# Kernel tuning notes

Measured on AMD Instinct MI355X. Metric: run time of the kernel, lower is better.

The kernel has to match this reference:

```python
import jax, jax.numpy as jnp
import numpy as np

N_NODES = 100000
N_EDGES = 3200000
N_FEAT = 512
HIDDEN = 16
N_CLASSES = 40


def gcn_conv(x, src, dst, W, b, num_nodes):
    # GCNConv with self-loops and symmetric normalization (default PyG settings).
    loop = jnp.arange(num_nodes)
    s = jnp.concatenate([src, loop])
    d = jnp.concatenate([dst, loop])
    deg = jax.ops.segment_sum(jnp.ones_like(s, dtype=x.dtype), d, num_segments=num_nodes)
    dinv = jnp.where(deg > 0, jax.lax.rsqrt(deg), 0.0)
    norm = dinv[s] * dinv[d]  # [E+N]
    h = x @ W  # [N, out]
    msg = h[s] * norm[:, None]  # gather + scale
    out = jax.ops.segment_sum(msg, d, num_segments=num_nodes)  # scatter-add
    return out + b


def setup_inputs() -> dict:
    key = jax.random.key(0)
    k1, k2, k3, k4 = jax.random.split(key, 4)
    x = jax.random.normal(k1, (N_NODES, N_FEAT), dtype=jnp.float32)
    edge_index = jax.random.randint(k2, (2, N_EDGES), 0, N_NODES, dtype=jnp.int64)
    W1 = jax.random.normal(k3, (N_FEAT, HIDDEN), dtype=jnp.float32) * 0.05
    b1 = jnp.zeros((HIDDEN,), dtype=jnp.float32)
    W2 = jax.random.normal(k4, (HIDDEN, N_CLASSES), dtype=jnp.float32) * 0.05
    b2 = jnp.zeros((N_CLASSES,), dtype=jnp.float32)
    return {"x": x, "edge_index": edge_index, "W1": W1, "b1": b1, "W2": W2, "b2": b2}


def reference(x, edge_index, W1, b1, W2, b2):
    num_nodes = x.shape[0]
    src, dst = edge_index[0], edge_index[1]
    h = gcn_conv(x, src, dst, W1, b1, num_nodes)
    h = jax.nn.relu(h)
    # dropout is identity in eval mode (training=False)
    out = gcn_conv(h, src, dst, W2, b2, num_nodes)
    return jax.nn.log_softmax(out, axis=1)
```

## Files before the change

kernel.cpp:

```cpp
#include <hip/hip_runtime.h>

#define N_NODES 100000
#define N_EDGES 3200000
#define N_FEAT 512
#define HIDDEN 16
#define N_CLASSES 40

#define SCAN_BLOCKS 98


__global__ void k_zero_int(int* p, int n) {
    int i = blockIdx.x * 256 + threadIdx.x;
    if (i < n) p[i] = 0;
}

__global__ void k_count(const int* __restrict__ dst, int* __restrict__ cnt,
                        int* __restrict__ ord) {
    int e = blockIdx.x * 256 + threadIdx.x;
    if (e < N_EDGES) ord[e] = atomicAdd(cnt + dst[e], 1);
}

__global__ void k_dinv(const int* __restrict__ cnt, float* __restrict__ dinv) {
    int i = blockIdx.x * 256 + threadIdx.x;
    if (i < N_NODES) dinv[i] = rsqrtf((float)(cnt[i] + 1));
}


__global__ __launch_bounds__(1024) void k_scan_a(const int* __restrict__ cnt,
                                                 int* __restrict__ bsum) {
    int tid = threadIdx.x;
    int i = blockIdx.x * 1024 + tid;
    int v = (i < N_NODES) ? cnt[i] : 0;
    #pragma unroll
    for (int off = 32; off >= 1; off >>= 1) v += __shfl_xor(v, off, 64);
    __shared__ int ws[16];
    if ((tid & 63) == 0) ws[tid >> 6] = v;
    __syncthreads();
    if (tid == 0) {
        int s = 0;
        #pragma unroll
        for (int w = 0; w < 16; w++) s += ws[w];
        bsum[blockIdx.x] = s;
    }
}

__global__ __launch_bounds__(128) void k_scan_b(const int* __restrict__ bsum,
                                                int* __restrict__ boff) {
    int tid = threadIdx.x;
    int lane = tid & 63, wv = tid >> 6;
    int v = (tid < SCAN_BLOCKS) ? bsum[tid] : 0;
    int sc = v;
    #pragma unroll
    for (int off = 1; off < 64; off <<= 1) {
        int t = __shfl_up(sc, off, 64);
        if (lane >= off) sc += t;
    }
    __shared__ int wsum[2];
    if (lane == 63) wsum[wv] = sc;
    __syncthreads();
    int pre = (wv == 1) ? wsum[0] : 0;
    if (tid < SCAN_BLOCKS) boff[tid] = pre + sc - v;
}

__global__ __launch_bounds__(1024) void k_scan_c(const int* __restrict__ cnt,
                                                 const int* __restrict__ boff,
                                                 int* __restrict__ row_start) {
    int tid = threadIdx.x;
    int i = blockIdx.x * 1024 + tid;
    int lane = tid & 63, wv = tid >> 6;
    int v = (i < N_NODES) ? cnt[i] : 0;
    int sc = v;
    #pragma unroll
    for (int off = 1; off < 64; off <<= 1) {
        int t = __shfl_up(sc, off, 64);
        if (lane >= off) sc += t;
    }
    __shared__ int wsum[16];
    if (lane == 63) wsum[wv] = sc;
    __syncthreads();
    int pre = 0;
    #pragma unroll
    for (int w = 0; w < 16; w++) pre += (w < wv) ? wsum[w] : 0;
    int excl = boff[blockIdx.x] + pre + sc - v;
    if (i < N_NODES) row_start[i] = excl;
    if (i == N_NODES) row_start[N_NODES] = N_EDGES;
}

__global__ void k_build(const int* __restrict__ src, const int* __restrict__ dst,
                        const int* __restrict__ ord, const int* __restrict__ row_start,
                        const float* __restrict__ dinv, int2* __restrict__ edge_data) {
    int e = blockIdx.x * 256 + threadIdx.x;
    if (e >= N_EDGES) return;
    int s = src[e], d = dst[e];
    int slot = row_start[d] + ord[e];
    float nrm = dinv[s] * dinv[d];
    edge_data[slot] = make_int2(s, __float_as_int(nrm));
}


#define KC 32
#define LDSW 36

__global__ __launch_bounds__(256) void k_gemm1(const float* __restrict__ x,
                                               const float* __restrict__ W1,
                                               float* __restrict__ h1) {
    __shared__ float xs[256 * LDSW];
    int tid = threadIdx.x;
    int row = blockIdx.x * 256 + tid;

    float acc[HIDDEN];
    #pragma unroll
    for (int j = 0; j < HIDDEN; j++) acc[j] = 0.f;

    int s_sub = tid >> 3;
    int s_k4  = tid & 7;

    for (int kc = 0; kc < N_FEAT; kc += KC) {
        __syncthreads();
        #pragma unroll
        for (int l = 0; l < 8; l++) {
            int srow = s_sub + l * 32;
            int grow = blockIdx.x * 256 + srow;
            int gr = grow < N_NODES ? grow : N_NODES - 1;
            float4 v = *reinterpret_cast<const float4*>(
                x + (size_t)gr * N_FEAT + kc + s_k4 * 4);
            *reinterpret_cast<float4*>(&xs[srow * LDSW + s_k4 * 4]) = v;
        }
        __syncthreads();

        const float* Wc = W1 + kc * HIDDEN;
        #pragma unroll
        for (int k4 = 0; k4 < 8; k4++) {
            float4 xv = *reinterpret_cast<const float4*>(&xs[tid * LDSW + k4 * 4]);
            const float* w0 = Wc + (k4 * 4 + 0) * HIDDEN;
            const float* w1 = Wc + (k4 * 4 + 1) * HIDDEN;
            const float* w2 = Wc + (k4 * 4 + 2) * HIDDEN;
            const float* w3 = Wc + (k4 * 4 + 3) * HIDDEN;
            #pragma unroll
            for (int j = 0; j < HIDDEN; j++) {
                acc[j] += xv.x * w0[j];
                acc[j] += xv.y * w1[j];
                acc[j] += xv.z * w2[j];
                acc[j] += xv.w * w3[j];
            }
        }
    }

    if (row < N_NODES) {
        float4* op = reinterpret_cast<float4*>(h1 + (size_t)row * HIDDEN);
        #pragma unroll
        for (int q = 0; q < 4; q++)
            op[q] = make_float4(acc[q*4+0], acc[q*4+1], acc[q*4+2], acc[q*4+3]);
    }
}


template <bool RELU>
__global__ __launch_bounds__(256) void k_agg16(const int2* __restrict__ edge_data,
                                               const int* __restrict__ row_start,
                                               const float* __restrict__ dinv,
                                               const float* __restrict__ h,
                                               const float* __restrict__ bias,
                                               float* __restrict__ out) {
    int g = threadIdx.x >> 4, j = threadIdx.x & 15;
    int node = blockIdx.x * 16 + g;
    if (node >= N_NODES) return;
    int beg = row_start[node], end = row_start[node + 1];
    float ds = dinv[node];
    float acc = h[(size_t)node * HIDDEN + j] * (ds * ds);
    int i = beg;
    for (; i + 3 < end; i += 4) {
        int2 e0 = edge_data[i + 0];
        int2 e1 = edge_data[i + 1];
        int2 e2 = edge_data[i + 2];
        int2 e3 = edge_data[i + 3];
        float v0 = h[(size_t)e0.x * HIDDEN + j];
        float v1 = h[(size_t)e1.x * HIDDEN + j];
        float v2 = h[(size_t)e2.x * HIDDEN + j];
        float v3 = h[(size_t)e3.x * HIDDEN + j];
        acc += v0 * __int_as_float(e0.y);
        acc += v1 * __int_as_float(e1.y);
        acc += v2 * __int_as_float(e2.y);
        acc += v3 * __int_as_float(e3.y);
    }
    for (; i < end; ++i) {
        int2 ed = edge_data[i];
        acc += h[(size_t)ed.x * HIDDEN + j] * __int_as_float(ed.y);
    }
    if (RELU) acc = fmaxf(acc + bias[j], 0.f);
    out[(size_t)node * HIDDEN + j] = acc;
}


__global__ __launch_bounds__(256) void k_out(const float* __restrict__ agg2,
                                             const float* __restrict__ W2,
                                             const float* __restrict__ b2,
                                             float* __restrict__ out) {
    int r = blockIdx.x * 256 + threadIdx.x;
    if (r >= N_NODES) return;
    float a[HIDDEN];
    const float4* ap = reinterpret_cast<const float4*>(agg2 + (size_t)r * HIDDEN);
    #pragma unroll
    for (int q = 0; q < 4; q++) {
        float4 v = ap[q];
        a[q * 4 + 0] = v.x; a[q * 4 + 1] = v.y;
        a[q * 4 + 2] = v.z; a[q * 4 + 3] = v.w;
    }
    float acc[N_CLASSES];
    #pragma unroll
    for (int jj = 0; jj < N_CLASSES; jj++) acc[jj] = b2[jj];
    #pragma unroll
    for (int kk = 0; kk < HIDDEN; kk++) {
        float av = a[kk];
        #pragma unroll
        for (int jj = 0; jj < N_CLASSES; jj++)
            acc[jj] += av * W2[kk * N_CLASSES + jj];
    }
    float m = -1e30f;
    #pragma unroll
    for (int jj = 0; jj < N_CLASSES; jj++) m = fmaxf(m, acc[jj]);
    float sum = 0.f;
    #pragma unroll
    for (int jj = 0; jj < N_CLASSES; jj++) sum += __expf(acc[jj] - m);
    float l = m + __logf(sum);
    float4* op = reinterpret_cast<float4*>(out + (size_t)r * N_CLASSES);
    #pragma unroll
    for (int q = 0; q < N_CLASSES / 4; q++) {
        op[q] = make_float4(acc[q*4+0] - l, acc[q*4+1] - l,
                            acc[q*4+2] - l, acc[q*4+3] - l);
    }
}


extern "C" void kernel_launch(void* const* d_in, const int* in_sizes, int n_in,
                              void* d_out, int out_size, void* d_ws, size_t ws_size,
                              hipStream_t stream) {
    const float* x  = (const float*)d_in[0];
    const int*   ei = (const int*)d_in[1];
    const float* W1 = (const float*)d_in[2];
    const float* b1 = (const float*)d_in[3];
    const float* W2 = (const float*)d_in[4];
    const float* b2 = (const float*)d_in[5];
    const int* src = ei;
    const int* dst = ei + N_EDGES;
    float* out = (float*)d_out;

    char* ws = (char*)d_ws;
    size_t off = 0;
    auto alloc = [&](size_t bytes) {
        size_t o = off; off = (off + bytes + 255) & ~(size_t)255; return o;
    };
    float* dinv      = (float*)(ws + alloc(sizeof(float) * N_NODES));
    int*   cnt       = (int*)  (ws + alloc(sizeof(int) * N_NODES));
    int*   row_start = (int*)  (ws + alloc(sizeof(int) * (N_NODES + 1)));
    int*   ord       = (int*)  (ws + alloc(sizeof(int) * N_EDGES));
    int2*  edge_data = (int2*) (ws + alloc(sizeof(int2) * N_EDGES));
    float* h1        = (float*)(ws + alloc(sizeof(float) * N_NODES * HIDDEN));
    float* rbuf      = (float*)(ws + alloc(sizeof(float) * N_NODES * HIDDEN));
    float* agg2      = (float*)(ws + alloc(sizeof(float) * N_NODES * HIDDEN));
    int*   bsum      = (int*)  (ws + alloc(sizeof(int) * SCAN_BLOCKS));
    int*   boff      = (int*)  (ws + alloc(sizeof(int) * SCAN_BLOCKS));

    const int nodeBlocks  = (N_NODES + 255) / 256;
    const int edgeBlocks  = (N_EDGES + 255) / 256;
    const int aggBlocks   = (N_NODES + 15) / 16;

    k_zero_int<<<nodeBlocks, 256, 0, stream>>>(cnt, N_NODES);
    k_count<<<edgeBlocks, 256, 0, stream>>>(dst, cnt, ord);
    k_dinv<<<nodeBlocks, 256, 0, stream>>>(cnt, dinv);
    k_scan_a<<<SCAN_BLOCKS, 1024, 0, stream>>>(cnt, bsum);
    k_scan_b<<<1, 128, 0, stream>>>(bsum, boff);
    k_scan_c<<<SCAN_BLOCKS, 1024, 0, stream>>>(cnt, boff, row_start);
    k_build<<<edgeBlocks, 256, 0, stream>>>(src, dst, ord, row_start, dinv, edge_data);

    k_gemm1<<<nodeBlocks, 256, 0, stream>>>(x, W1, h1);
    k_agg16<true><<<aggBlocks, 256, 0, stream>>>(edge_data, row_start, dinv, h1, b1, rbuf);
    k_agg16<false><<<aggBlocks, 256, 0, stream>>>(edge_data, row_start, dinv, rbuf, nullptr, agg2);
    k_out<<<nodeBlocks, 256, 0, stream>>>(agg2, W2, b2, out);
}
```

Measured before the change: 677.1 us.

## Privatize degree counters per XCD with workgroup-scope atomics

```diff
diff --git a/kernel.cpp b/kernel.cpp
--- a/kernel.cpp
+++ b/kernel.cpp
@@ -5,6 +5,7 @@
 #define N_FEAT 512
 #define HIDDEN 16
 #define N_CLASSES 40
+#define NXCD 8
 
 #define SCAN_BLOCKS 98
 
@@ -14,15 +15,36 @@
     if (i < n) p[i] = 0;
 }
 
-__global__ void k_count(const int* __restrict__ dst, int* __restrict__ cnt,
+__device__ __forceinline__ int xcc_id() {
+    int x;
+    asm("s_getreg_b32 %0, hwreg(HW_REG_XCC_ID)" : "=s"(x));
+    return x & (NXCD - 1);
+}
+
+__global__ void k_count(const int* __restrict__ dst, int* __restrict__ cnt8,
                         int* __restrict__ ord) {
     int e = blockIdx.x * 256 + threadIdx.x;
-    if (e < N_EDGES) ord[e] = atomicAdd(cnt + dst[e], 1);
-}
-
-__global__ void k_dinv(const int* __restrict__ cnt, float* __restrict__ dinv) {
+    if (e >= N_EDGES) return;
+    int c = xcc_id();
+    int d = dst[e];
+    int o = __hip_atomic_fetch_add(cnt8 + c * N_NODES + d, 1,
+                                   __ATOMIC_RELAXED, __HIP_MEMORY_SCOPE_WORKGROUP);
+    ord[e] = (o << 3) | c;
+}
+
+__global__ void k_merge(int* __restrict__ cnt8, int* __restrict__ cnt,
+                        float* __restrict__ dinv) {
     int i = blockIdx.x * 256 + threadIdx.x;
-    if (i < N_NODES) dinv[i] = rsqrtf((float)(cnt[i] + 1));
+    if (i >= N_NODES) return;
+    int s = 0;
+    #pragma unroll
+    for (int c = 0; c < NXCD; c++) {
+        int v = cnt8[c * N_NODES + i];
+        cnt8[c * N_NODES + i] = s;
+        s += v;
+    }
+    cnt[i] = s;
+    dinv[i] = rsqrtf((float)(s + 1));
 }
 
 
@@ -88,11 +110,14 @@
 
 __global__ void k_build(const int* __restrict__ src, const int* __restrict__ dst,
                         const int* __restrict__ ord, const int* __restrict__ row_start,
-                        const float* __restrict__ dinv, int2* __restrict__ edge_data) {
+                        const int* __restrict__ cnt8, const float* __restrict__ dinv,
+                        int2* __restrict__ edge_data) {
     int e = blockIdx.x * 256 + threadIdx.x;
     if (e >= N_EDGES) return;
     int s = src[e], d = dst[e];
-    int slot = row_start[d] + ord[e];
+    int oc = ord[e];
+    int c = oc & (NXCD - 1), o = oc >> 3;
+    int slot = row_start[d] + cnt8[c * N_NODES + d] + o;
     float nrm = dinv[s] * dinv[d];
     edge_data[slot] = make_int2(s, __float_as_int(nrm));
 }
@@ -260,18 +285,20 @@
     float* agg2      = (float*)(ws + alloc(sizeof(float) * N_NODES * HIDDEN));
     int*   bsum      = (int*)  (ws + alloc(sizeof(int) * SCAN_BLOCKS));
     int*   boff      = (int*)  (ws + alloc(sizeof(int) * SCAN_BLOCKS));
+    int*   cnt8      = (int*)agg2;
 
     const int nodeBlocks  = (N_NODES + 255) / 256;
     const int edgeBlocks  = (N_EDGES + 255) / 256;
     const int aggBlocks   = (N_NODES + 15) / 16;
-
-    k_zero_int<<<nodeBlocks, 256, 0, stream>>>(cnt, N_NODES);
-    k_count<<<edgeBlocks, 256, 0, stream>>>(dst, cnt, ord);
-    k_dinv<<<nodeBlocks, 256, 0, stream>>>(cnt, dinv);
+    const int zero8Blocks = (NXCD * N_NODES + 255) / 256;
+
+    k_zero_int<<<zero8Blocks, 256, 0, stream>>>(cnt8, NXCD * N_NODES);
+    k_count<<<edgeBlocks, 256, 0, stream>>>(dst, cnt8, ord);
+    k_merge<<<nodeBlocks, 256, 0, stream>>>(cnt8, cnt, dinv);
     k_scan_a<<<SCAN_BLOCKS, 1024, 0, stream>>>(cnt, bsum);
     k_scan_b<<<1, 128, 0, stream>>>(bsum, boff);
     k_scan_c<<<SCAN_BLOCKS, 1024, 0, stream>>>(cnt, boff, row_start);
-    k_build<<<edgeBlocks, 256, 0, stream>>>(src, dst, ord, row_start, dinv, edge_data);
+    k_build<<<edgeBlocks, 256, 0, stream>>>(src, dst, ord, row_start, cnt8, dinv, edge_data);
 
     k_gemm1<<<nodeBlocks, 256, 0, stream>>>(x, W1, h1);
     k_agg16<true><<<aggBlocks, 256, 0, stream>>>(edge_data, row_start, dinv, h1, b1, rbuf);
```

New measurement: 690.7 us. 1.02x slower.

## Build CSR with LDS-partitioned histogram counting and bucketed placement

Applied to the files above, without the earlier changes.

```diff
diff --git a/kernel.cpp b/kernel.cpp
--- a/kernel.cpp
+++ b/kernel.cpp
@@ -8,21 +8,49 @@
 
 #define SCAN_BLOCKS 98
 
-
-__global__ void k_zero_int(int* p, int n) {
-    int i = blockIdx.x * 256 + threadIdx.x;
-    if (i < n) p[i] = 0;
-}
-
-__global__ void k_count(const int* __restrict__ dst, int* __restrict__ cnt,
-                        int* __restrict__ ord) {
-    int e = blockIdx.x * 256 + threadIdx.x;
-    if (e < N_EDGES) ord[e] = atomicAdd(cnt + dst[e], 1);
-}
-
-__global__ void k_dinv(const int* __restrict__ cnt, float* __restrict__ dinv) {
-    int i = blockIdx.x * 256 + threadIdx.x;
-    if (i < N_NODES) dinv[i] = rsqrtf((float)(cnt[i] + 1));
+#define CH    16384
+#define NCH   7
+#define NS    32
+#define SLICE (N_EDGES / NS)
+#define SL4   (SLICE / 4)
+
+__global__ __launch_bounds__(512) void k_p1(const int* __restrict__ dst,
+                                            int* __restrict__ partS) {
+    __shared__ int hist[CH];
+    int tid = threadIdx.x;
+    int s = blockIdx.x, j = blockIdx.y;
+    int base = j * CH;
+    int lim = N_NODES - base; if (lim > CH) lim = CH;
+    for (int i = tid; i < CH; i += 512) hist[i] = 0;
+    __syncthreads();
+    const int4* dp = reinterpret_cast<const int4*>(dst + s * SLICE);
+    for (int i = tid; i < SL4; i += 512) {
+        int4 d4 = dp[i];
+        unsigned a = (unsigned)(d4.x - base); if (a < (unsigned)lim) atomicAdd(&hist[a], 1);
+        unsigned b = (unsigned)(d4.y - base); if (b < (unsigned)lim) atomicAdd(&hist[b], 1);
+        unsigned c = (unsigned)(d4.z - base); if (c < (unsigned)lim) atomicAdd(&hist[c], 1);
+        unsigned d = (unsigned)(d4.w - base); if (d < (unsigned)lim) atomicAdd(&hist[d], 1);
+    }
+    __syncthreads();
+    for (int i = tid; i < lim; i += 512)
+        partS[s * N_NODES + base + i] = hist[i];
+}
+
+__global__ __launch_bounds__(256) void k_colscan(int* __restrict__ partS,
+                                                 int* __restrict__ deg,
+                                                 float* __restrict__ dinv) {
+    int n = blockIdx.x * 256 + threadIdx.x;
+    if (n >= N_NODES) return;
+    int run = 0;
+    #pragma unroll
+    for (int s = 0; s < NS; s++) {
+        int idx = s * N_NODES + n;
+        int v = partS[idx];
+        partS[idx] = run;
+        run += v;
+    }
+    deg[n] = run;
+    dinv[n] = rsqrtf((float)(run + 1));
 }
 
 
@@ -86,15 +114,54 @@
     if (i == N_NODES) row_start[N_NODES] = N_EDGES;
 }
 
-__global__ void k_build(const int* __restrict__ src, const int* __restrict__ dst,
-                        const int* __restrict__ ord, const int* __restrict__ row_start,
-                        const float* __restrict__ dinv, int2* __restrict__ edge_data) {
-    int e = blockIdx.x * 256 + threadIdx.x;
-    if (e >= N_EDGES) return;
-    int s = src[e], d = dst[e];
-    int slot = row_start[d] + ord[e];
-    float nrm = dinv[s] * dinv[d];
-    edge_data[slot] = make_int2(s, __float_as_int(nrm));
+__global__ __launch_bounds__(512) void k_p2(const int* __restrict__ src,
+                                            const int* __restrict__ dst,
+                                            const int* __restrict__ partS,
+                                            const int* __restrict__ row_start,
+                                            const float* __restrict__ dinv,
+                                            int2* __restrict__ edge_data) {
+    __shared__ int cur[CH];
+    int tid = threadIdx.x;
+    int s = blockIdx.x, j = blockIdx.y;
+    int base = j * CH;
+    int lim = N_NODES - base; if (lim > CH) lim = CH;
+    for (int i = tid; i < lim; i += 512)
+        cur[i] = row_start[base + i] + partS[s * N_NODES + base + i];
+    __syncthreads();
+    const int4* dp = reinterpret_cast<const int4*>(dst + s * SLICE);
+    const int4* sp = reinterpret_cast<const int4*>(src + s * SLICE);
+    for (int i = tid; i < SL4; i += 512) {
+        int4 d4 = dp[i];
+        int4 s4 = sp[i];
+        {
+            unsigned nl = (unsigned)(d4.x - base);
+            if (nl < (unsigned)lim) {
+                int slot = atomicAdd(&cur[nl], 1);
+                edge_data[slot] = make_int2(s4.x, __float_as_int(dinv[s4.x] * dinv[d4.x]));
+            }
+        }
+        {
+            unsigned nl = (unsigned)(d4.y - base);
+            if (nl < (unsigned)lim) {
+                int slot = atomicAdd(&cur[nl], 1);
+                edge_data[slot] = make_int2(s4.y, __float_as_int(dinv[s4.y] * dinv[d4.y]));
+            }
+        }
+        {
+            unsigned nl = (unsigned)(d4.z - base);
+            if (nl < (unsigned)lim) {
+                int slot = atomicAdd(&cur[nl], 1);
+                edge_data[slot] = make_int2(s4.z, __float_as_int(dinv[s4.z] * dinv[d4.z]));
+            }
+        }
+        {
+            unsigned nl = (unsigned)(d4.w - base);
+            if (nl < (unsigned)lim) {
+                int slot = atomicAdd(&cur[nl], 1);
+                edge_data[slot] = make_int2(s4.w, __float_as_int(dinv[s4.w] * dinv[d4.w]));
+            }
+        }
+    }
 }
 
 
@@ -253,7 +320,7 @@
     float* dinv      = (float*)(ws + alloc(sizeof(float) * N_NODES));
     int*   cnt       = (int*)  (ws + alloc(sizeof(int) * N_NODES));
     int*   row_start = (int*)  (ws + alloc(sizeof(int) * (N_NODES + 1)));
-    int*   ord       = (int*)  (ws + alloc(sizeof(int) * N_EDGES));
+    int*   partS     = (int*)  (ws + alloc(sizeof(int) * (size_t)NS * N_NODES));
     int2*  edge_data = (int2*) (ws + alloc(sizeof(int2) * N_EDGES));
     float* h1        = (float*)(ws + alloc(sizeof(float) * N_NODES * HIDDEN));
     float* rbuf      = (float*)(ws + alloc(sizeof(float) * N_NODES * HIDDEN));
@@ -262,16 +329,15 @@
     int*   boff      = (int*)  (ws + alloc(sizeof(int) * SCAN_BLOCKS));
 
     const int nodeBlocks  = (N_NODES + 255) / 256;
-    const int edgeBlocks  = (N_EDGES + 255) / 256;
     const int aggBlocks   = (N_NODES + 15) / 16;
-
-    k_zero_int<<<nodeBlocks, 256, 0, stream>>>(cnt, N_NODES);
-    k_count<<<edgeBlocks, 256, 0, stream>>>(dst, cnt, ord);
-    k_dinv<<<nodeBlocks, 256, 0, stream>>>(cnt, dinv);
+    dim3 csGrid(NS, NCH);
+
+    k_p1<<<csGrid, 512, 0, stream>>>(dst, partS);
+    k_colscan<<<nodeBlocks, 256, 0, stream>>>(partS, cnt, dinv);
     k_scan_a<<<SCAN_BLOCKS, 1024, 0, stream>>>(cnt, bsum);
     k_scan_b<<<1, 128, 0, stream>>>(bsum, boff);
     k_scan_c<<<SCAN_BLOCKS, 1024, 0, stream>>>(cnt, boff, row_start);
-    k_build<<<edgeBlocks, 256, 0, stream>>>(src, dst, ord, row_start, dinv, edge_data);
+    k_p2<<<csGrid, 512, 0, stream>>>(src, dst, partS, row_start, dinv, edge_data);
 
     k_gemm1<<<nodeBlocks, 256, 0, stream>>>(x, W1, h1);
     k_agg16<true><<<aggBlocks, 256, 0, stream>>>(edge_data, row_start, dinv, h1, b1, rbuf);
```

After: 621.1 us. 1.09x faster.
